# Kernel optimization log

Hardware: AMD Instinct MI355X
Metric: run time of the kernel (lower is better)

The kernel has to match this reference:

```python
import jax, jax.numpy as jnp
import numpy as np

NUM = 21  # classes 1..NUM scored; bin 0 is background, bin NUM+1 is a dump bin


def _class_counts(y_pred, y_true):
    # Single-pass histogram over all classes instead of O(num) full-tensor scans.
    yp = y_pred.ravel()
    yt = y_true.ravel()
    nbins = NUM + 2
    cnt_true = jnp.zeros((nbins,), jnp.float32).at[yt].add(1.0)
    cnt_pred = jnp.zeros((nbins,), jnp.float32).at[yp].add(1.0)
    # intersection: positions where pred == true, binned by label; mismatches -> dump bin
    inter_idx = jnp.where(yp == yt, yt, NUM + 1)
    inter = jnp.zeros((nbins,), jnp.float32).at[inter_idx].add(1.0)
    return cnt_true, cnt_pred, inter


def setup_inputs() -> dict:
    key = jax.random.key(0)
    k1, k2 = jax.random.split(key)
    shape = (32, 1024, 1024)
    y_pred = jax.random.randint(k1, shape, 0, NUM + 1, dtype=jnp.int32)
    y_true = jax.random.randint(k2, shape, 0, NUM + 1, dtype=jnp.int32)
    return {"y_pred": y_pred, "y_true": y_true}


def reference(y_pred, y_true):
    cnt_true, cnt_pred, inter = _class_counts(y_pred, y_true)
    # classes 1..NUM (label 0 skipped, as in the original loop over range(1, num+1))
    c_true = cnt_true[1:NUM + 1]
    c_pred = cnt_pred[1:NUM + 1]
    c_inter = inter[1:NUM + 1]
    union = c_true + c_pred - c_inter
    iou = (c_inter + 1e-6) / (union + 1e-6)  # [NUM]
    present = (c_true > 0).astype(jnp.float32)
    mIoU = jnp.sum(iou * present) / jnp.maximum(jnp.sum(present), 1.0)
    return mIoU, iou
```

## Files before the change

### kernel.cpp

```cpp
#include <hip/hip_runtime.h>


#define NUMC  21
#define NBINS 22
#define JBINS (NBINS * NBINS)
#define RSTR  485
#define NREP  4
#define GRID  2048

typedef int iv4 __attribute__((ext_vector_type(4)));

__global__ void __launch_bounds__(256) hist_joint(
        const int* __restrict__ yp, const int* __restrict__ yt,
        unsigned int* __restrict__ partials, int n) {
    __shared__ unsigned int h[NREP * RSTR];
    for (int i = threadIdx.x; i < NREP * RSTR; i += 256) h[i] = 0u;
    __syncthreads();

    unsigned int* hh = h + (threadIdx.x >> 6) * RSTR;

    const iv4* __restrict__ yp4 = (const iv4*)yp;
    const iv4* __restrict__ yt4 = (const iv4*)yt;
    const int n4 = n >> 2;
    const int stride = GRID * 256;
    int i = blockIdx.x * 256 + threadIdx.x;

#define DS4(P, T)                                      \
    atomicAdd(&hh[(T).x * NBINS + (P).x], 1u);         \
    atomicAdd(&hh[(T).y * NBINS + (P).y], 1u);         \
    atomicAdd(&hh[(T).z * NBINS + (P).z], 1u);         \
    atomicAdd(&hh[(T).w * NBINS + (P).w], 1u);

    if (i < n4) {
        iv4 p = __builtin_nontemporal_load(yp4 + i);
        iv4 t = __builtin_nontemporal_load(yt4 + i);
        int j = i + stride;
        for (; j < n4; j += stride) {
            iv4 pn = __builtin_nontemporal_load(yp4 + j);
            iv4 tn = __builtin_nontemporal_load(yt4 + j);
            DS4(p, t)
            p = pn; t = tn;
        }
        DS4(p, t)
    }
#undef DS4

    if (blockIdx.x == 0 && threadIdx.x == 0) {
        for (int k = n4 << 2; k < n; k++)
            atomicAdd(&hh[yt[k] * NBINS + yp[k]], 1u);
    }

    __syncthreads();
    for (int c = threadIdx.x; c < JBINS; c += 256) {
        unsigned int s = h[c] + h[RSTR + c] + h[2 * RSTR + c] + h[3 * RSTR + c];
        partials[(size_t)blockIdx.x * JBINS + c] = s;
    }
}

__global__ void __launch_bounds__(256) reduce_partials(
        const unsigned int* __restrict__ partials,
        unsigned int* __restrict__ g, int nblocks) {
    __shared__ unsigned int lds[256];
    const int c = blockIdx.x;
    unsigned int s = 0;
    for (int b = threadIdx.x; b < nblocks; b += 256)
        s += partials[(size_t)b * JBINS + c];
    lds[threadIdx.x] = s;
    __syncthreads();
    for (int w = 128; w > 0; w >>= 1) {
        if (threadIdx.x < w) lds[threadIdx.x] += lds[threadIdx.x + w];
        __syncthreads();
    }
    if (threadIdx.x == 0) g[c] = lds[0];
}

__global__ void finalize_kernel(const unsigned int* __restrict__ g,
                                float* __restrict__ out) {
    int lane = threadIdx.x;
    float iou = 0.0f, pres = 0.0f;
    if (lane >= 1 && lane <= NUMC) {
        unsigned int ct = 0, cp = 0;
        #pragma unroll
        for (int k = 0; k < NBINS; k++) {
            ct += g[lane * NBINS + k];
            cp += g[k * NBINS + lane];
        }
        unsigned int ci = g[lane * NBINS + lane];
        float u = (float)ct + (float)cp - (float)ci;
        iou = ((float)ci + 1e-6f) / (u + 1e-6f);
        pres = (ct > 0u) ? 1.0f : 0.0f;
        out[lane] = iou;
    }
    float v = iou * pres, pc = pres;
    #pragma unroll
    for (int off = 32; off > 0; off >>= 1) {
        v += __shfl_down(v, off);
        pc += __shfl_down(pc, off);
    }
    if (lane == 0) out[0] = v / fmaxf(pc, 1.0f);
}

extern "C" void kernel_launch(void* const* d_in, const int* in_sizes, int n_in,
                              void* d_out, int out_size, void* d_ws, size_t ws_size,
                              hipStream_t stream) {
    const int* yp = (const int*)d_in[0];
    const int* yt = (const int*)d_in[1];
    int n = in_sizes[0];
    float* out = (float*)d_out;

    unsigned int* g = (unsigned int*)d_ws;
    unsigned int* partials = g + JBINS;

    hist_joint<<<GRID, 256, 0, stream>>>(yp, yt, partials, n);
    reduce_partials<<<JBINS, 256, 0, stream>>>(partials, g, GRID);
    finalize_kernel<<<1, 64, 0, stream>>>(g, out);
}
```

Before: 260.6 us.

## Stage input via global_load_lds double buffering and merge partials with global atomics

Replaces register-prefetched nontemporal loads with asynchronous global-to-LDS loads into a per-wave double buffer, waited on with explicit waitcnt, for the evenly divisible case. Halves the number of LDS histogram replicas, so two waves share one copy. Drops the separate partial-reduction kernel: each block atomically adds its nonzero bins into a global histogram that is zeroed with a memset. This removes a kernel launch and the partials traffic, but adds more LDS atomic contention, extra LDS use for staging, and global atomic traffic at the end of each block.

Result: slower. 274.0 us (+5.2%).

```diff
diff --git a/kernel.cpp b/kernel.cpp
--- a/kernel.cpp
+++ b/kernel.cpp
@@ -5,25 +5,16 @@
 #define NBINS 22
 #define JBINS (NBINS * NBINS)
 #define RSTR  485
-#define NREP  4
+#define NREP  2
 #define GRID  2048
+#define TPB   256
 
 typedef int iv4 __attribute__((ext_vector_type(4)));
 
-__global__ void __launch_bounds__(256) hist_joint(
-        const int* __restrict__ yp, const int* __restrict__ yt,
-        unsigned int* __restrict__ partials, int n) {
-    __shared__ unsigned int h[NREP * RSTR];
-    for (int i = threadIdx.x; i < NREP * RSTR; i += 256) h[i] = 0u;
-    __syncthreads();
-
-    unsigned int* hh = h + (threadIdx.x >> 6) * RSTR;
-
-    const iv4* __restrict__ yp4 = (const iv4*)yp;
-    const iv4* __restrict__ yt4 = (const iv4*)yt;
-    const int n4 = n >> 2;
-    const int stride = GRID * 256;
-    int i = blockIdx.x * 256 + threadIdx.x;
+#define GLDS(GP, LP) \
+    __builtin_amdgcn_global_load_lds( \
+        (const __attribute__((address_space(1))) void*)(GP), \
+        (__attribute__((address_space(3))) void*)(LP), 16, 0, 2)
 
 #define DS4(P, T)                                      \
     atomicAdd(&hh[(T).x * NBINS + (P).x], 1u);         \
@@ -31,47 +22,72 @@
     atomicAdd(&hh[(T).z * NBINS + (P).z], 1u);         \
     atomicAdd(&hh[(T).w * NBINS + (P).w], 1u);
 
-    if (i < n4) {
-        iv4 p = __builtin_nontemporal_load(yp4 + i);
-        iv4 t = __builtin_nontemporal_load(yt4 + i);
-        int j = i + stride;
-        for (; j < n4; j += stride) {
-            iv4 pn = __builtin_nontemporal_load(yp4 + j);
-            iv4 tn = __builtin_nontemporal_load(yt4 + j);
+__global__ void __launch_bounds__(256) hist_joint(
+        const int* __restrict__ yp, const int* __restrict__ yt,
+        unsigned int* __restrict__ g, int n) {
+    __shared__ unsigned int hist[NREP * RSTR];
+    __shared__ __align__(16) int stage[4  * 4 * 256];
+
+    for (int i = threadIdx.x; i < NREP * RSTR; i += TPB) hist[i] = 0u;
+    __syncthreads();
+
+    const int lane = threadIdx.x & 63;
+    const int wave = threadIdx.x >> 6;
+    unsigned int* hh = hist + (wave >> 1) * RSTR;
+
+    const iv4* __restrict__ yp4 = (const iv4*)yp;
+    const iv4* __restrict__ yt4 = (const iv4*)yt;
+    const int n4 = n >> 2;
+    const int stride = GRID * TPB;
+    const int i0 = blockIdx.x * TPB + threadIdx.x;
+    const int iters = n4 / stride;
+
+    if (iters * stride == n4 && (n & 3) == 0) {
+        int* base = stage + wave * 1024;
+        int* bp[2] = { base,       base + 512 };
+        int* bt[2] = { base + 256, base + 768 };
+
+        GLDS(yp4 + i0, bp[0]);
+        GLDS(yt4 + i0, bt[0]);
+
+        for (int it = 0; it < iters; ++it) {
+            const int b = it & 1;
+            if (it + 1 < iters) {
+                const int j = i0 + (it + 1) * stride;
+                GLDS(yp4 + j, bp[b ^ 1]);
+                GLDS(yt4 + j, bt[b ^ 1]);
+                __builtin_amdgcn_s_waitcnt(0x0F72);
+            } else {
+                __builtin_amdgcn_s_waitcnt(0x0F70);
+            }
+            __builtin_amdgcn_sched_barrier(0);
+            iv4 p = *((const iv4*)bp[b] + lane);
+            iv4 t = *((const iv4*)bt[b] + lane);
             DS4(p, t)
-            p = pn; t = tn;
         }
-        DS4(p, t)
-    }
-#undef DS4
-
-    if (blockIdx.x == 0 && threadIdx.x == 0) {
-        for (int k = n4 << 2; k < n; k++)
-            atomicAdd(&hh[yt[k] * NBINS + yp[k]], 1u);
+    } else {
+        if (i0 < n4) {
+            iv4 p = __builtin_nontemporal_load(yp4 + i0);
+            iv4 t = __builtin_nontemporal_load(yt4 + i0);
+            for (int j = i0 + stride; j < n4; j += stride) {
+                iv4 pn = __builtin_nontemporal_load(yp4 + j);
+                iv4 tn = __builtin_nontemporal_load(yt4 + j);
+                DS4(p, t)
+                p = pn; t = tn;
+            }
+            DS4(p, t)
+        }
+        if (blockIdx.x == 0 && threadIdx.x == 0) {
+            for (int k = n4 << 2; k < n; k++)
+                atomicAdd(&hh[yt[k] * NBINS + yp[k]], 1u);
+        }
     }
 
     __syncthreads();
-    for (int c = threadIdx.x; c < JBINS; c += 256) {
-        unsigned int s = h[c] + h[RSTR + c] + h[2 * RSTR + c] + h[3 * RSTR + c];
-        partials[(size_t)blockIdx.x * JBINS + c] = s;
+    for (int c = threadIdx.x; c < JBINS; c += TPB) {
+        unsigned int s = hist[c] + hist[RSTR + c];
+        if (s) atomicAdd(&g[c], s);
     }
-}
-
-__global__ void __launch_bounds__(256) reduce_partials(
-        const unsigned int* __restrict__ partials,
-        unsigned int* __restrict__ g, int nblocks) {
-    __shared__ unsigned int lds[256];
-    const int c = blockIdx.x;
-    unsigned int s = 0;
-    for (int b = threadIdx.x; b < nblocks; b += 256)
-        s += partials[(size_t)b * JBINS + c];
-    lds[threadIdx.x] = s;
-    __syncthreads();
-    for (int w = 128; w > 0; w >>= 1) {
-        if (threadIdx.x < w) lds[threadIdx.x] += lds[threadIdx.x + w];
-        __syncthreads();
-    }
-    if (threadIdx.x == 0) g[c] = lds[0];
 }
 
 __global__ void finalize_kernel(const unsigned int* __restrict__ g,
@@ -107,11 +123,9 @@
     const int* yt = (const int*)d_in[1];
     int n = in_sizes[0];
     float* out = (float*)d_out;
+    unsigned int* g = (unsigned int*)d_ws;
 
-    unsigned int* g = (unsigned int*)d_ws;
-    unsigned int* partials = g + JBINS;
-
-    hist_joint<<<GRID, 256, 0, stream>>>(yp, yt, partials, n);
-    reduce_partials<<<JBINS, 256, 0, stream>>>(partials, g, GRID);
+    hipMemsetAsync(g, 0, JBINS * sizeof(unsigned int), stream);
+    hist_joint<<<GRID, TPB, 0, stream>>>(yp, yt, g, n);
     finalize_kernel<<<1, 64, 0, stream>>>(g, out);
 }
```
